# Kernel optimization log

Measured on AMD Instinct MI355X. Metric: run time of the kernel, lower is better.

The kernel has to match this reference:

```python
import jax, jax.numpy as jnp
from jax import lax
import numpy as np

# GatedLinearAttention: S_t = alpha_t * S_{t-1} + k_t^T v_t ; o_t = q_t @ S_t
DIM = 1024
H = 8
DK = 128   # dim*expand_k(1.0)/H
DV = 256   # dim*expand_v(2.0)/H
GATE_NORM = 16.0

def setup_inputs() -> dict:
    key = jax.random.key(0)
    ks = jax.random.split(key, 8)
    B, S = 2, 4096
    def xavier(k, shape, gain=1.0):
        fan_in, fan_out = shape[0], shape[1]
        lim = gain * np.sqrt(6.0 / (fan_in + fan_out))
        return jax.random.uniform(k, shape, jnp.float32, -lim, lim)
    g = 2 ** (-2.5)
    # weights stored as [in, out] so y = x @ W (transpose of torch Linear storage)
    return {
        "x":   jax.random.normal(ks[0], (B, S, DIM), jnp.float32),
        "Wq":  xavier(ks[1], (DIM, H * DK), g),
        "Wk":  xavier(ks[2], (DIM, H * DK), g),
        "Wv":  xavier(ks[3], (DIM, H * DV), g),
        "Wo":  xavier(ks[4], (H * DV, DIM)),
        "Wg":  xavier(ks[5], (DIM, H)),
        "bg":  jnp.zeros((H,), jnp.float32),
        "Wog": xavier(ks[6], (DIM, H * DV)),
    }

def _gla(x, Wq, Wk, Wv, Wo, Wg, bg, Wog):
    B, S, D = x.shape
    q = (x @ Wq).reshape(B, S, H, DK)
    k = (x @ Wk).reshape(B, S, H, DK) * (DK ** -0.5)
    v = (x @ Wv).reshape(B, S, H, DV)
    alpha = jax.nn.sigmoid((x @ Wg + bg) / GATE_NORM)  # [B,S,H]

    def step(state, inp):
        qt, kt, vt, at = inp  # [B,H,dk], [B,H,dk], [B,H,dv], [B,H]
        state = at[..., None, None] * state + kt[..., None] * vt[:, :, None, :]
        out_t = jnp.einsum('bhk,bhkv->bhv', qt, state)
        return state, out_t

    state0 = jnp.zeros((B, H, DK, DV), x.dtype)
    xs = (jnp.moveaxis(q, 1, 0), jnp.moveaxis(k, 1, 0),
          jnp.moveaxis(v, 1, 0), jnp.moveaxis(alpha, 1, 0))
    _, outs = lax.scan(step, state0, xs)          # [S,B,H,dv]
    out = jnp.moveaxis(outs, 0, 1).reshape(B, S, H * DV)
    og = jax.nn.sigmoid(x @ Wog)
    return (out * og) @ Wo

def reference(x, Wq, Wk, Wv, Wo, Wg, bg, Wog):
    return _gla(x, Wq, Wk, Wv, Wo, Wg, bg, Wog)
```

## Files before the change

### kernel.cpp

```cpp
#include <hip/hip_runtime.h>
#include <cstdint>
#include <cstddef>

typedef unsigned short u16;
typedef unsigned int   u32;
typedef __attribute__((ext_vector_type(8))) short short8;
typedef __attribute__((ext_vector_type(4))) float f32x4;

__device__ __forceinline__ u16 f2bf(float f) {
    union { float f; u32 u; } v; v.f = f;
    u32 r = v.u + 0x7fffu + ((v.u >> 16) & 1u);
    return (u16)(r >> 16);
}
__device__ __forceinline__ float bf2f(u16 b) {
    union { u32 u; float f; } v; v.u = ((u32)b) << 16;
    return v.f;
}

__device__ __forceinline__ void gload16(const u16* g, u16* l) {
    __builtin_amdgcn_global_load_lds(
        (const __attribute__((address_space(1))) u32*)g,
        (__attribute__((address_space(3))) u32*)l,
        16, 0, 0);
}

#define SEQ   4096
#define BATCH 2
#define NH    8
#define DKH   128
#define DVH   256
#define DMODEL 1024
#define NPROJ 6144
#define CHUNK 64
#define NCHUNK (SEQ / CHUNK)

#define OFF_XB    0u
#define OFF_WCAT  16777216u
#define OFF_WOT   29360128u
#define OFF_PROJ  33554432u
#define OFF_L2A   134217728u
#define OFF_GC    134479872u
#define OFF_U     134483968u
#define OFF_Z     201592832u

__global__ __launch_bounds__(256) void cvt_x_kernel(const float* __restrict__ x,
                                                    u16* __restrict__ xb) {
    int i = (blockIdx.x * 256 + threadIdx.x) * 4;
    float4 v = *(const float4*)(x + i);
    u16 o[4] = { f2bf(v.x), f2bf(v.y), f2bf(v.z), f2bf(v.w) };
    *(uint2*)(xb + i) = *(const uint2*)o;
}

__global__ __launch_bounds__(256) void transpose_w(const float* __restrict__ W, int N, int K,
                                                   u16* __restrict__ outp, float scale) {
    __shared__ float t[32][33];
    int n0 = blockIdx.x * 32, k0 = blockIdx.y * 32;
    int tx = threadIdx.x, ty = threadIdx.y;
    #pragma unroll
    for (int j = 0; j < 4; ++j)
        t[ty + j * 8][tx] = W[(size_t)(k0 + ty + j * 8) * N + n0 + tx];
    __syncthreads();
    #pragma unroll
    for (int j = 0; j < 4; ++j)
        outp[(size_t)(n0 + ty + j * 8) * K + k0 + tx] = f2bf(t[tx][ty + j * 8] * scale);
}

__global__ __launch_bounds__(256) void alpha_kernel(const float* __restrict__ x,
                                                    const float* __restrict__ Wg,
                                                    const float* __restrict__ bg,
                                                    float* __restrict__ l2a) {
    __shared__ float xr[DMODEL];
    int row = blockIdx.x;
    for (int i = threadIdx.x; i < DMODEL; i += 256) xr[i] = x[(size_t)row * DMODEL + i];
    __syncthreads();
    int wave = threadIdx.x >> 6, lane = threadIdx.x & 63;
    #pragma unroll
    for (int hh = 0; hh < 2; ++hh) {
        int h = wave * 2 + hh;
        float p = 0.f;
        for (int i = lane; i < DMODEL; i += 64) p += xr[i] * Wg[i * NH + h];
        #pragma unroll
        for (int d = 32; d; d >>= 1) p += __shfl_down(p, d, 64);
        if (lane == 0) {
            float zz = (p + bg[h]) * (1.0f / 16.0f);
            float a = 1.0f / (1.0f + expf(-zz));
            l2a[row * NH + h] = log2f(a);
        }
    }
}

template <int EPI>
__global__ __launch_bounds__(256) void gemm_glds(const u16* __restrict__ A, int lda,
                                                 const u16* __restrict__ B, int ldb,
                                                 void* __restrict__ Cout, int ldc,
                                                 int K, int og_start) {
    __shared__ u16 smem[18432];
    u16* As = smem;
    u16* Bs = smem + 4096;
    const int tid = threadIdx.x;
    const int lane = tid & 63, wave = tid >> 6;
    const int m0 = blockIdx.y * 128, n0 = blockIdx.x * 128;
    const int m_off = (wave & 1) * 64, n_off = (wave >> 1) * 64;
    const int r = tid >> 2, kg = (tid & 3) * 8;
    f32x4 acc[4][4] = {};
    for (int k0 = 0; k0 < K; k0 += 32) {
        #pragma unroll
        for (int i = 0; i < 2; ++i) {
            int row = i * 64 + r;
            gload16(A + (size_t)(m0 + row) * lda + k0 + kg, As + (i * 256 + (tid & 192)) * 8);
            gload16(B + (size_t)(n0 + row) * ldb + k0 + kg, Bs + (i * 256 + (tid & 192)) * 8);
        }
        __syncthreads();
        short8 a[4], b[4];
        #pragma unroll
        for (int rt = 0; rt < 4; ++rt)
            a[rt] = *reinterpret_cast<const short8*>(&As[(m_off + rt * 16 + (lane & 15)) * 32 + (lane >> 4) * 8]);
        #pragma unroll
        for (int ct = 0; ct < 4; ++ct)
            b[ct] = *reinterpret_cast<const short8*>(&Bs[(n_off + ct * 16 + (lane & 15)) * 32 + (lane >> 4) * 8]);
        #pragma unroll
        for (int rt = 0; rt < 4; ++rt)
            #pragma unroll
            for (int ct = 0; ct < 4; ++ct)
                acc[rt][ct] = __builtin_amdgcn_mfma_f32_16x16x32_bf16(a[rt], b[ct], acc[rt][ct], 0, 0, 0);
        __syncthreads();
    }
    if (EPI) {
        u16* Cw = smem + wave * 4608;
        #pragma unroll
        for (int rt = 0; rt < 4; ++rt)
            #pragma unroll
            for (int ct = 0; ct < 4; ++ct)
                #pragma unroll
                for (int j = 0; j < 4; ++j) {
                    int row = rt * 16 + (lane >> 4) * 4 + j;
                    int col = ct * 16 + (lane & 15);
                    int n = n0 + n_off + col;
                    float v = acc[rt][ct][j];
                    if (n >= og_start) v = 1.0f / (1.0f + expf(-v));
                    Cw[row * 72 + col] = f2bf(v);
                }
        #pragma unroll
        for (int it = 0; it < 8; ++it) {
            int row = it * 8 + (lane >> 3);
            int c8 = (lane & 7) * 8;
            uint4 val = *reinterpret_cast<const uint4*>(&Cw[row * 72 + c8]);
            *reinterpret_cast<uint4*>((u16*)Cout + (size_t)(m0 + m_off + row) * ldc + n0 + n_off + c8) = val;
        }
    } else {
        #pragma unroll
        for (int rt = 0; rt < 4; ++rt)
            #pragma unroll
            for (int ct = 0; ct < 4; ++ct)
                #pragma unroll
                for (int j = 0; j < 4; ++j) {
                    int m = m0 + m_off + rt * 16 + (lane >> 4) * 4 + j;
                    int n = n0 + n_off + ct * 16 + (lane & 15);
                    ((float*)Cout)[(size_t)m * ldc + n] = acc[rt][ct][j];
                }
    }
}

__global__ __launch_bounds__(256) void r1_kernel(const u16* __restrict__ proj,
                                                 const float* __restrict__ l2a,
                                                 u16* __restrict__ U,
                                                 float* __restrict__ Gc) {
    __shared__ u16 kT[128 * 72];
    __shared__ u16 vT[256 * 72];
    __shared__ float Wsh[64];
    int bid = blockIdx.x;
    int c = bid & 63, bh = bid >> 6;
    int b = bh >> 3, h = bh & 7;
    int c0 = c * CHUNK;
    int tid = threadIdx.x, lane = tid & 63, wave = tid >> 6;
    size_t rowbase = (size_t)b * SEQ + c0;
    if (wave == 0) {
        float L = l2a[(rowbase + lane) * NH + h];
        #pragma unroll
        for (int d = 1; d < 64; d <<= 1) {
            float u = __shfl_up(L, d, 64);
            if (lane >= d) L += u;
        }
        float Lend = __shfl(L, 63, 64);
        Wsh[lane] = exp2f(Lend - L);
        if (lane == 0) Gc[bh * NCHUNK + c] = exp2f(Lend);
    }
    __syncthreads();
    #pragma unroll
    for (int j = 0; j < 4; ++j) {
        int cid = tid + j * 256;
        int s = cid >> 4, r = (cid & 15) * 8;
        uint4 v = *(const uint4*)(proj + (rowbase + s) * NPROJ + 1024 + h * DKH + r);
        u16 e[8]; *(uint4*)e = v;
        #pragma unroll
        for (int i = 0; i < 8; ++i) kT[(r + i) * 72 + s] = e[i];
    }
    #pragma unroll
    for (int j = 0; j < 8; ++j) {
        int cid = tid + j * 256;
        int s = cid >> 5, cc = (cid & 31) * 8;
        float w = Wsh[s];
        uint4 v = *(const uint4*)(proj + (rowbase + s) * NPROJ + 2048 + h * DVH + cc);
        u16 e[8]; *(uint4*)e = v;
        #pragma unroll
        for (int i = 0; i < 8; ++i) vT[(cc + i) * 72 + s] = f2bf(bf2f(e[i]) * w);
    }
    __syncthreads();
    short8 afr[4][2];
    #pragma unroll
    for (int rt = 0; rt < 4; ++rt)
        #pragma unroll
        for (int kk = 0; kk < 2; ++kk)
            afr[rt][kk] = *reinterpret_cast<const short8*>(
                &vT[(wave * 64 + rt * 16 + (lane & 15)) * 72 + kk * 32 + (lane >> 4) * 8]);
    size_t ubase = (size_t)(bh * NCHUNK + c) * (DVH * DKH);
    #pragma unroll
    for (int ct = 0; ct < 8; ++ct) {
        f32x4 acc[4] = {};
        #pragma unroll
        for (int kk = 0; kk < 2; ++kk) {
            short8 bfr = *reinterpret_cast<const short8*>(
                &kT[(ct * 16 + (lane & 15)) * 72 + kk * 32 + (lane >> 4) * 8]);
            #pragma unroll
            for (int rt = 0; rt < 4; ++rt)
                acc[rt] = __builtin_amdgcn_mfma_f32_16x16x32_bf16(afr[rt][kk], bfr, acc[rt], 0, 0, 0);
        }
        #pragma unroll
        for (int rt = 0; rt < 4; ++rt)
            #pragma unroll
            for (int j = 0; j < 4; ++j) {
                int ccr = wave * 64 + rt * 16 + (lane >> 4) * 4 + j;
                int rr = ct * 16 + (lane & 15);
                U[ubase + (size_t)ccr * DKH + rr] = f2bf(acc[rt][j]);
            }
    }
}

__global__ __launch_bounds__(256) void r2_kernel(u16* __restrict__ U, const float* __restrict__ Gc) {
    int bh = blockIdx.x >> 5;
    int e0 = ((blockIdx.x & 31) * 256 + threadIdx.x) * 4;
    const float* g = Gc + bh * NCHUNK;
    size_t base = (size_t)bh * NCHUNK * (DVH * DKH) + e0;
    float s0 = 0.f, s1 = 0.f, s2 = 0.f, s3 = 0.f;
    for (int c = 0; c < NCHUNK; ++c) {
        u16* p = U + base + (size_t)c * (DVH * DKH);
        uint2 u = *(const uint2*)p;
        u16 e[4]; *(uint2*)e = u;
        u16 o[4] = { f2bf(s0), f2bf(s1), f2bf(s2), f2bf(s3) };
        *(uint2*)p = *(const uint2*)o;
        float G = g[c];
        s0 = G * s0 + bf2f(e[0]);
        s1 = G * s1 + bf2f(e[1]);
        s2 = G * s2 + bf2f(e[2]);
        s3 = G * s3 + bf2f(e[3]);
    }
}

__global__ __launch_bounds__(256) void r3_kernel(const u16* __restrict__ proj,
                                                 const u16* __restrict__ Sp,
                                                 const float* __restrict__ l2a,
                                                 u16* __restrict__ z) {
    __shared__ u16 vT[256 * 72];
    __shared__ u16 P[64 * 72];
    __shared__ float Lsh[64];
    int bid = blockIdx.x;
    int c = bid & 63, bh = bid >> 6;
    int b = bh >> 3, h = bh & 7;
    int c0 = c * CHUNK;
    int tid = threadIdx.x, lane = tid & 63, wave = tid >> 6;
    size_t rowbase = (size_t)b * SEQ + c0;
    if (wave == 0) {
        float L = l2a[(rowbase + lane) * NH + h];
        #pragma unroll
        for (int d = 1; d < 64; d <<= 1) {
            float u = __shfl_up(L, d, 64);
            if (lane >= d) L += u;
        }
        Lsh[lane] = L;
    }
    #pragma unroll
    for (int j = 0; j < 8; ++j) {
        int cid = tid + j * 256;
        int s = cid >> 5, cc = (cid & 31) * 8;
        uint4 v = *(const uint4*)(proj + (rowbase + s) * NPROJ + 2048 + h * DVH + cc);
        u16 e[8]; *(uint4*)e = v;
        #pragma unroll
        for (int i = 0; i < 8; ++i) vT[(cc + i) * 72 + s] = e[i];
    }
    __syncthreads();
    {
        f32x4 pacc[4] = {};
        #pragma unroll
        for (int kk = 0; kk < 4; ++kk) {
            short8 a = *reinterpret_cast<const short8*>(
                proj + (rowbase + wave * 16 + (lane & 15)) * NPROJ + h * DKH + kk * 32 + (lane >> 4) * 8);
            #pragma unroll
            for (int st = 0; st < 4; ++st) {
                short8 bb = *reinterpret_cast<const short8*>(
                    proj + (rowbase + st * 16 + (lane & 15)) * NPROJ + 1024 + h * DKH + kk * 32 + (lane >> 4) * 8);
                pacc[st] = __builtin_amdgcn_mfma_f32_16x16x32_bf16(a, bb, pacc[st], 0, 0, 0);
            }
        }
        #pragma unroll
        for (int st = 0; st < 4; ++st)
            #pragma unroll
            for (int j = 0; j < 4; ++j) {
                int t = wave * 16 + (lane >> 4) * 4 + j;
                int s = st * 16 + (lane & 15);
                float val = pacc[st][j];
                val = (s <= t) ? val * exp2f(Lsh[t] - Lsh[s]) : 0.f;
                P[t * 72 + s] = f2bf(val);
            }
    }
    f32x4 acc[4][4] = {};
    size_t spbase = (size_t)(bh * NCHUNK + c) * (DVH * DKH);
    #pragma unroll
    for (int kk = 0; kk < 4; ++kk) {
        short8 a[4];
        #pragma unroll
        for (int rt = 0; rt < 4; ++rt)
            a[rt] = *reinterpret_cast<const short8*>(
                proj + (rowbase + rt * 16 + (lane & 15)) * NPROJ + h * DKH + kk * 32 + (lane >> 4) * 8);
        #pragma unroll
        for (int ct = 0; ct < 4; ++ct) {
            short8 bb = *reinterpret_cast<const short8*>(
                Sp + spbase + (size_t)(wave * 64 + ct * 16 + (lane & 15)) * DKH + kk * 32 + (lane >> 4) * 8);
            #pragma unroll
            for (int rt = 0; rt < 4; ++rt)
                acc[rt][ct] = __builtin_amdgcn_mfma_f32_16x16x32_bf16(a[rt], bb, acc[rt][ct], 0, 0, 0);
        }
    }
    #pragma unroll
    for (int rt = 0; rt < 4; ++rt)
        #pragma unroll
        for (int j = 0; j < 4; ++j) {
            float at = exp2f(Lsh[rt * 16 + (lane >> 4) * 4 + j]);
            #pragma unroll
            for (int ct = 0; ct < 4; ++ct) acc[rt][ct][j] *= at;
        }
    __syncthreads();
    #pragma unroll
    for (int kk = 0; kk < 2; ++kk) {
        short8 pa[4];
        #pragma unroll
        for (int rt = 0; rt < 4; ++rt)
            pa[rt] = *reinterpret_cast<const short8*>(&P[(rt * 16 + (lane & 15)) * 72 + kk * 32 + (lane >> 4) * 8]);
        #pragma unroll
        for (int ct = 0; ct < 4; ++ct) {
            short8 vb = *reinterpret_cast<const short8*>(
                &vT[(wave * 64 + ct * 16 + (lane & 15)) * 72 + kk * 32 + (lane >> 4) * 8]);
            #pragma unroll
            for (int rt = 0; rt < 4; ++rt)
                acc[rt][ct] = __builtin_amdgcn_mfma_f32_16x16x32_bf16(pa[rt], vb, acc[rt][ct], 0, 0, 0);
        }
    }
    #pragma unroll
    for (int rt = 0; rt < 4; ++rt)
        #pragma unroll
        for (int ct = 0; ct < 4; ++ct)
            #pragma unroll
            for (int j = 0; j < 4; ++j) {
                int t = rt * 16 + (lane >> 4) * 4 + j;
                int cc = wave * 64 + ct * 16 + (lane & 15);
                float og = bf2f(proj[(rowbase + t) * NPROJ + 4096 + h * DVH + cc]);
                float v = acc[rt][ct][j] * og;
                z[(rowbase + t) * (NH * DVH) + h * DVH + cc] = f2bf(v);
            }
}

extern "C" void kernel_launch(void* const* d_in, const int* in_sizes, int n_in,
                              void* d_out, int out_size, void* d_ws, size_t ws_size,
                              hipStream_t stream) {
    const float* x   = (const float*)d_in[0];
    const float* Wq  = (const float*)d_in[1];
    const float* Wk  = (const float*)d_in[2];
    const float* Wv  = (const float*)d_in[3];
    const float* Wo  = (const float*)d_in[4];
    const float* Wg  = (const float*)d_in[5];
    const float* bg  = (const float*)d_in[6];
    const float* Wog = (const float*)d_in[7];
    float* out = (float*)d_out;
    char* ws = (char*)d_ws;

    u16*   xb   = (u16*)(ws + OFF_XB);
    u16*   wcat = (u16*)(ws + OFF_WCAT);
    u16*   wot  = (u16*)(ws + OFF_WOT);
    u16*   proj = (u16*)(ws + OFF_PROJ);
    float* l2a  = (float*)(ws + OFF_L2A);
    float* gc   = (float*)(ws + OFF_GC);
    u16*   U    = (u16*)(ws + OFF_U);
    u16*   z    = (u16*)(ws + OFF_Z);

    cvt_x_kernel<<<8192, 256, 0, stream>>>(x, xb);
    dim3 tb(32, 8);
    transpose_w<<<dim3(32, 32), tb, 0, stream>>>(Wq,  1024, 1024, wcat,               1.0f);
    transpose_w<<<dim3(32, 32), tb, 0, stream>>>(Wk,  1024, 1024, wcat + 1024 * 1024, 0.08838834764831845f);
    transpose_w<<<dim3(64, 32), tb, 0, stream>>>(Wv,  2048, 1024, wcat + 2048 * 1024, 1.0f);
    transpose_w<<<dim3(64, 32), tb, 0, stream>>>(Wog, 2048, 1024, wcat + 4096 * 1024, 1.0f);
    transpose_w<<<dim3(32, 64), tb, 0, stream>>>(Wo,  1024, 2048, wot,                1.0f);
    alpha_kernel<<<8192, 256, 0, stream>>>(x, Wg, bg, l2a);
    gemm_glds<1><<<dim3(48, 64), 256, 0, stream>>>(xb, 1024, wcat, 1024, proj, NPROJ, 1024, 4096);
    r1_kernel<<<BATCH * NH * NCHUNK, 256, 0, stream>>>(proj, l2a, U, gc);
    r2_kernel<<<512, 256, 0, stream>>>(U, gc);
    r3_kernel<<<BATCH * NH * NCHUNK, 256, 0, stream>>>(proj, U, l2a, z);
    gemm_glds<0><<<dim3(8, 64), 256, 0, stream>>>(z, 2048, wot, 2048, out, 1024, 2048, 1 << 30);
}
```

Baseline: 608.0 us.

## Replace projection GEMM with 256x256-tile, 512-thread pipelined kernel

Adds a new GEMM kernel with 256x256 output tiles, 8 waves, a 4-stage LDS ring with two tiles of prefetch, XOR-swizzled LDS layout, and an XCD-aware block remapping. The fused QKV/gate projection GEMM now uses it instead of the 128x128 kernel. The goal is more reuse per loaded tile and better overlap of global loads with MFMA work. In exchange it uses 128 KB of LDS and a large accumulator register footprint, which limits occupancy.

```diff
diff --git a/kernel.cpp b/kernel.cpp
--- a/kernel.cpp
+++ b/kernel.cpp
@@ -86,6 +86,114 @@
             float a = 1.0f / (1.0f + expf(-zz));
             l2a[row * NH + h] = log2f(a);
         }
+    }
+}
+
+template <int EPI>
+__global__ __launch_bounds__(512, 2) void gemm256(const u16* __restrict__ A, int lda,
+                                                  const u16* __restrict__ B, int ldb,
+                                                  void* __restrict__ Cout, int ldc,
+                                                  int K, int nTN, int og_start) {
+    __shared__ u16 lds[65536];
+    const int tid = threadIdx.x;
+    const int lane = tid & 63, wid = tid >> 6;
+    const int wr = wid >> 2, wc = wid & 3;
+    const int cpx = gridDim.x >> 3;
+    const int wg = (blockIdx.x & 7) * cpx + (blockIdx.x >> 3);
+    const int m0 = (wg / nTN) * 256, n0 = (wg % nTN) * 256;
+
+    const int rsub = tid >> 2;
+    const int ql = (tid & 3) ^ ((tid >> 4) & 3);
+    const size_t ag0 = (size_t)(m0 + rsub) * lda + ql * 8;
+    const size_t ag1 = (size_t)(m0 + 128 + rsub) * lda + ql * 8;
+    const size_t bg0 = (size_t)(n0 + rsub) * ldb + ql * 8;
+    const size_t bg1 = (size_t)(n0 + 128 + rsub) * ldb + ql * 8;
+    const int sdw = wid * 512;
+
+#define STG_A(t_, h_) gload16(A + ((h_) ? ag1 : ag0) + (size_t)(t_) * 32, \
+                              lds + ((t_) & 3) * 8192 + (h_) * 4096 + sdw)
+#define STG_B(t_, h_) gload16(B + ((h_) ? bg1 : bg0) + (size_t)(t_) * 32, \
+                              lds + 32768 + ((t_) & 3) * 8192 + (h_) * 4096 + sdw)
+
+    const int qr = ((lane >> 4) ^ ((lane >> 2) & 3)) * 8;
+    const int arow = (wr * 128 + (lane & 15)) * 32 + qr;
+    const int brow = 32768 + (wc * 64 + (lane & 15)) * 32 + qr;
+
+    STG_A(0, 0); STG_A(0, 1); STG_B(0, 0); STG_B(0, 1);
+    STG_A(1, 0); STG_A(1, 1); STG_B(1, 0); STG_B(1, 1);
+    asm volatile("s_waitcnt vmcnt(4)\n\ts_barrier" ::: "memory");
+
+    f32x4 acc[8][4] = {};
+    const int NT = K >> 5;
+    for (int t = 0; t < NT; ++t) {
+        const u16* buf = lds + (t & 3) * 8192;
+        const bool pre = (t + 2) < NT;
+        if (pre) { STG_A(t + 2, 0); STG_A(t + 2, 1); }
+        short8 bfr[4], afr[4];
+        #pragma unroll
+        for (int ct = 0; ct < 4; ++ct) bfr[ct] = *(const short8*)(buf + brow + ct * 512);
+        #pragma unroll
+        for (int rt = 0; rt < 4; ++rt) afr[rt] = *(const short8*)(buf + arow + rt * 512);
+        __builtin_amdgcn_s_setprio(1);
+        #pragma unroll
+        for (int rt = 0; rt < 4; ++rt)
+            #pragma unroll
+            for (int ct = 0; ct < 4; ++ct)
+                acc[rt][ct] = __builtin_amdgcn_mfma_f32_16x16x32_bf16(afr[rt], bfr[ct], acc[rt][ct], 0, 0, 0);
+        __builtin_amdgcn_s_setprio(0);
+        if (pre) { STG_B(t + 2, 0); STG_B(t + 2, 1); }
+        #pragma unroll
+        for (int rt = 0; rt < 4; ++rt) afr[rt] = *(const short8*)(buf + arow + (rt + 4) * 512);
+        __builtin_amdgcn_s_setprio(1);
+        #pragma unroll
+        for (int rt = 0; rt < 4; ++rt)
+            #pragma unroll
+            for (int ct = 0; ct < 4; ++ct)
+                acc[rt + 4][ct] = __builtin_amdgcn_mfma_f32_16x16x32_bf16(afr[rt], bfr[ct], acc[rt + 4][ct], 0, 0, 0);
+        __builtin_amdgcn_s_setprio(0);
+        if (t < NT - 2)       asm volatile("s_waitcnt vmcnt(4)\n\ts_barrier" ::: "memory");
+        else if (t == NT - 2) asm volatile("s_waitcnt vmcnt(0)\n\ts_barrier" ::: "memory");
+    }
+#undef STG_A
+#undef STG_B
+
+    __syncthreads();
+    if (EPI) {
+        u16* Cw = lds + wid * 4608;
+        #pragma unroll
+        for (int pass = 0; pass < 2; ++pass) {
+            #pragma unroll
+            for (int rt = 0; rt < 4; ++rt)
+                #pragma unroll
+                for (int ct = 0; ct < 4; ++ct)
+                    #pragma unroll
+                    for (int j = 0; j < 4; ++j) {
+                        int row = rt * 16 + (lane >> 4) * 4 + j;
+                        int col = ct * 16 + (lane & 15);
+                        float v = acc[pass * 4 + rt][ct][j];
+                        if (n0 + wc * 64 + col >= og_start) v = 1.0f / (1.0f + expf(-v));
+                        Cw[row * 72 + col] = f2bf(v);
+                    }
+            #pragma unroll
+            for (int it = 0; it < 8; ++it) {
+                int row = it * 8 + (lane >> 3);
+                int c8 = (lane & 7) * 8;
+                uint4 val = *reinterpret_cast<const uint4*>(&Cw[row * 72 + c8]);
+                *reinterpret_cast<uint4*>((u16*)Cout +
+                    (size_t)(m0 + wr * 128 + pass * 64 + row) * ldc + n0 + wc * 64 + c8) = val;
+            }
+        }
+    } else {
+        #pragma unroll
+        for (int rt = 0; rt < 8; ++rt)
+            #pragma unroll
+            for (int ct = 0; ct < 4; ++ct)
+                #pragma unroll
+                for (int j = 0; j < 4; ++j) {
+                    int m = m0 + wr * 128 + rt * 16 + (lane >> 4) * 4 + j;
+                    int n = n0 + wc * 64 + ct * 16 + (lane & 15);
+                    ((float*)Cout)[(size_t)m * ldc + n] = acc[rt][ct][j];
+                }
     }
 }
 
@@ -399,7 +507,7 @@
     transpose_w<<<dim3(64, 32), tb, 0, stream>>>(Wog, 2048, 1024, wcat + 4096 * 1024, 1.0f);
     transpose_w<<<dim3(32, 64), tb, 0, stream>>>(Wo,  1024, 2048, wot,                1.0f);
     alpha_kernel<<<8192, 256, 0, stream>>>(x, Wg, bg, l2a);
-    gemm_glds<1><<<dim3(48, 64), 256, 0, stream>>>(xb, 1024, wcat, 1024, proj, NPROJ, 1024, 4096);
+    gemm256<1><<<768, 512, 0, stream>>>(xb, 1024, wcat, 1024, proj, NPROJ, 1024, 24, 4096);
     r1_kernel<<<BATCH * NH * NCHUNK, 256, 0, stream>>>(proj, l2a, U, gc);
     r2_kernel<<<512, 256, 0, stream>>>(U, gc);
     r3_kernel<<<BATCH * NH * NCHUNK, 256, 0, stream>>>(proj, U, l2a, z);
```

After: 586.5 us. 3.5% less time.
